# Kernel tuning notes

Hardware: AMD Instinct MI355X
Metric: run time of the kernel (lower is better)

Reference implementation:

```python
import jax, jax.numpy as jnp
import numpy as np

RADIUS, HEAD, SLOT, DIM = 16.0, 8, 112, 512

def _l2norm(x, axis):
    n = jnp.linalg.norm(x, axis=axis, keepdims=True)
    return x / jnp.maximum(n, 1e-12)

def _layernorm(x, g, b, eps=1e-5):
    mu = jnp.mean(x, axis=-1, keepdims=True)
    var = jnp.mean((x - mu) ** 2, axis=-1, keepdims=True)
    return (x - mu) / jnp.sqrt(var + eps) * g + b

def setup_inputs() -> dict:
    key = jax.random.key(0)
    ks = jax.random.split(key, 12)
    B, S = 32, 512
    return {
        "query": jax.random.normal(ks[0], (B, S, DIM), jnp.float32),
        "value": jax.random.normal(ks[1], (B, S, DIM), jnp.float32),
        "key_mem": jax.random.normal(ks[2], (HEAD * SLOT, DIM // HEAD), jnp.float32) * 0.5,
        "value_mem": jax.random.normal(ks[3], (SLOT, DIM), jnp.float32) * 0.5,
        "Wq": jax.random.normal(ks[4], (DIM, DIM), jnp.float32) * 0.02,
        "bq": jnp.zeros((DIM,), jnp.float32),
        "Wv": jax.random.normal(ks[5], (DIM, DIM), jnp.float32) * 0.02,
        "bv": jnp.zeros((DIM,), jnp.float32),
        "Wl": jax.random.normal(ks[6], (DIM, DIM * HEAD), jnp.float32) * 0.02,
        "bl": jnp.zeros((DIM,), jnp.float32),
        "g1": jnp.ones((DIM,), jnp.float32), "b1": jnp.zeros((DIM,), jnp.float32),
        "g2": jnp.ones((DIM,), jnp.float32), "b2": jnp.zeros((DIM,), jnp.float32),
        "g3": jnp.ones((DIM,), jnp.float32), "b3": jnp.zeros((DIM,), jnp.float32),
    }

def reference(query, value, key_mem, value_mem, Wq, bq, Wv, bv, Wl, bl,
              g1, b1, g2, b2, g3, b3):
    B, S, C = query.shape
    mq = query.reshape(B * S, C)                                   # (BS, 512)
    # --- key addressing (read path) ---
    key_norm = _l2norm(key_mem.reshape(HEAD, SLOT, -1), axis=2)    # (h, s, 64)
    eq = _l2norm((mq @ Wq.T + bq).reshape(B * S, HEAD, -1), axis=2)
    key_sim = jnp.einsum('bhd,hsd->bhs', eq, key_norm)             # (BS, h, s)
    key_add = jax.nn.softmax(RADIUS * key_sim, axis=2)
    m_head = jnp.einsum('bhs,sd->bhd', key_add,
                        jax.lax.stop_gradient(value_mem))          # (BS, h, 512)
    vir = _layernorm(m_head.reshape(B * S, HEAD * DIM) @ Wl.T + bl, g2, b2)
    te_fusion = _layernorm(query + vir.reshape(B, S, DIM), g1, b1)  # dropout = eval identity
    # --- value addressing (write/train path) ---
    mv = value.reshape(B * S, DIM)
    ev = jax.lax.stop_gradient(mv) @ Wv.T + bv
    value_norm = _l2norm(value_mem, axis=1)                        # (s, 512)
    value_sim = _l2norm(ev, axis=1) @ value_norm.T                 # (BS, s)
    value_add = jax.nn.softmax(RADIUS * value_sim, axis=1)
    aud = value_add @ value_mem                                    # (BS, 512)
    contrastive = 0.5 * jnp.abs(jnp.eye(SLOT, dtype=value_norm.dtype)
                                - value_norm @ value_norm.T).sum()[None]
    mvd = jax.lax.stop_gradient(mv)
    cos = (aud * mvd).sum(1) / jnp.maximum(
        jnp.linalg.norm(aud, axis=1) * jnp.linalg.norm(mvd, axis=1), 1e-8)
    recon = jnp.abs(1.0 - cos).reshape(B, S).sum(1)                # (B,)
    aud = _layernorm(aud, g3, b3)
    tr_fusion = _layernorm(query + aud.reshape(B, S, DIM), g1, b1)
    return (te_fusion, tr_fusion, recon, contrastive)
```

## Files before the change

kernel.cpp:

```cpp
#include <hip/hip_runtime.h>
#include <math.h>

#define DIMC   512
#define HEADS  8
#define SLOTS  112
#define HD     64
#define NROWS  16384
#define RADIUSF 16.0f

typedef short short8 __attribute__((ext_vector_type(8)));
typedef unsigned short ushort8 __attribute__((ext_vector_type(8)));
typedef float f32x4  __attribute__((ext_vector_type(4)));

__device__ __forceinline__ unsigned short f2bf(float f)
{
    unsigned u = __float_as_uint(f);
    unsigned r = (u + 0x7FFFu + ((u >> 16) & 1u)) >> 16;
    return (unsigned short)r;
}
__device__ __forceinline__ float bf2f(unsigned short h)
{
    return __uint_as_float((unsigned)h << 16);
}

__device__ __forceinline__ void gl16(const void* g, void* lds_wave_base)
{
    __builtin_amdgcn_global_load_lds(
        (const __attribute__((address_space(1))) unsigned int*)g,
        (__attribute__((address_space(3))) unsigned int*)lds_wave_base,
        16, 0, 0);
}

#define DPP_ADD(x, ctrl, rmask)                                               \
    (x) += __int_as_float(__builtin_amdgcn_update_dpp(                        \
               0, __float_as_int(x), (ctrl), (rmask), 0xf, true))

__device__ __forceinline__ float wsum64(float x)
{
    DPP_ADD(x, 0x111, 0xf);
    DPP_ADD(x, 0x112, 0xf);
    DPP_ADD(x, 0x114, 0xf);
    DPP_ADD(x, 0x118, 0xf);
    DPP_ADD(x, 0x142, 0xa);
    DPP_ADD(x, 0x143, 0xc);
    return __int_as_float(__builtin_amdgcn_readlane(__float_as_int(x), 63));
}

__device__ __forceinline__ void wsum64_4(float& a, float& b, float& c, float& d)
{
    DPP_ADD(a, 0x111, 0xf); DPP_ADD(b, 0x111, 0xf); DPP_ADD(c, 0x111, 0xf); DPP_ADD(d, 0x111, 0xf);
    DPP_ADD(a, 0x112, 0xf); DPP_ADD(b, 0x112, 0xf); DPP_ADD(c, 0x112, 0xf); DPP_ADD(d, 0x112, 0xf);
    DPP_ADD(a, 0x114, 0xf); DPP_ADD(b, 0x114, 0xf); DPP_ADD(c, 0x114, 0xf); DPP_ADD(d, 0x114, 0xf);
    DPP_ADD(a, 0x118, 0xf); DPP_ADD(b, 0x118, 0xf); DPP_ADD(c, 0x118, 0xf); DPP_ADD(d, 0x118, 0xf);
    DPP_ADD(a, 0x142, 0xa); DPP_ADD(b, 0x142, 0xa); DPP_ADD(c, 0x142, 0xa); DPP_ADD(d, 0x142, 0xa);
    DPP_ADD(a, 0x143, 0xc); DPP_ADD(b, 0x143, 0xc); DPP_ADD(c, 0x143, 0xc); DPP_ADD(d, 0x143, 0xc);
    a = __int_as_float(__builtin_amdgcn_readlane(__float_as_int(a), 63));
    b = __int_as_float(__builtin_amdgcn_readlane(__float_as_int(b), 63));
    c = __int_as_float(__builtin_amdgcn_readlane(__float_as_int(c), 63));
    d = __int_as_float(__builtin_amdgcn_readlane(__float_as_int(d), 63));
}

__global__ __launch_bounds__(256)
void gemm_bf16(const short* __restrict__ A, int lda,
               const short* __restrict__ B, int ldb,
               float* __restrict__ C, unsigned short* __restrict__ Cb,
               int ldc, int K, const float* __restrict__ bias, int Nvalid,
               int aZ, int bZ, int cZ)
{
    __shared__ short As[128 * 32];
    __shared__ short Bs[128 * 32];
    A += (size_t)blockIdx.z * aZ;
    B += (size_t)blockIdx.z * bZ;
    const size_t czoff = (size_t)blockIdx.z * cZ;
    const int tid  = threadIdx.x;
    const int wave = tid >> 6;
    const int lane = tid & 63;
    const int m0 = blockIdx.y * 128;
    const int n0 = blockIdx.x * 128;
    const int wm = (wave >> 1) * 64;
    const int wn = (wave & 1) * 64;

    const int srow = tid >> 2;
    const int schk = (tid & 3) * 8;

    const int fr = lane & 15;
    const int fq = (lane >> 4) * 8;

    f32x4 acc[4][4] = {};

    const short* Ag = A + (size_t)(m0 + srow) * lda + schk;
    const short* Bg = B + (size_t)(n0 + srow) * ldb + schk;

    short* asL = As + wave * 512;
    short* asU = As + 2048 + wave * 512;
    short* bsL = Bs + wave * 512;
    short* bsU = Bs + 2048 + wave * 512;

    for (int k0 = 0; k0 < K; k0 += 32) {
        gl16(Ag, asL);
        gl16(Ag + (size_t)64 * lda, asU);
        gl16(Bg, bsL);
        gl16(Bg + (size_t)64 * ldb, bsU);
        Ag += 32; Bg += 32;
        __syncthreads();
        short8 af[4], bf[4];
        #pragma unroll
        for (int i = 0; i < 4; ++i)
            af[i] = *(const short8*)&As[(wm + i * 16 + fr) * 32 + fq];
        #pragma unroll
        for (int j = 0; j < 4; ++j)
            bf[j] = *(const short8*)&Bs[(wn + j * 16 + fr) * 32 + fq];
        #pragma unroll
        for (int i = 0; i < 4; ++i)
            #pragma unroll
            for (int j = 0; j < 4; ++j)
                acc[i][j] = __builtin_amdgcn_mfma_f32_16x16x32_bf16(
                    af[i], bf[j], acc[i][j], 0, 0, 0);
        __syncthreads();
    }

    const int cr = (lane >> 4) * 4;
    const int cc = lane & 15;
    #pragma unroll
    for (int i = 0; i < 4; ++i) {
        const int grow = m0 + wm + i * 16 + cr;
        #pragma unroll
        for (int j = 0; j < 4; ++j) {
            const int gcol = n0 + wn + j * 16 + cc;
            if (gcol < Nvalid) {
                const float bb = bias ? bias[gcol] : 0.f;
                const size_t base = czoff + (size_t)grow * ldc + gcol;
                #pragma unroll
                for (int r = 0; r < 4; ++r) {
                    const float val = acc[i][j][r] + bb;
                    if (C)  C[base + (size_t)r * ldc]  = val;
                    if (Cb) Cb[base + (size_t)r * ldc] = f2bf(val);
                }
            }
        }
    }
}

__global__ __launch_bounds__(256)
void gemm_softmax(const short* __restrict__ A, int lda, int aZ,
                  const short* __restrict__ B, int ldb, int bZ,
                  int K,
                  unsigned short* __restrict__ Ob, int ldo, int oPerZ, int padN)
{
    __shared__ short As[128 * 32];
    __shared__ short Bs[128 * 32];
    __shared__ float P[128][113];
    __shared__ float hinvS[128];
    A += (size_t)blockIdx.z * aZ;
    B += (size_t)blockIdx.z * bZ;
    const int tid  = threadIdx.x;
    const int wave = tid >> 6;
    const int lane = tid & 63;
    const int m0 = blockIdx.y * 128;
    const int wm = (wave >> 1) * 64;
    const int wn = (wave & 1) * 64;
    const int srow = tid >> 2;
    const int schk = (tid & 3) * 8;
    const int fr = lane & 15;
    const int fq = (lane >> 4) * 8;

    f32x4 acc[4][4] = {};
    float ss[4] = {0.f, 0.f, 0.f, 0.f};

    const short* Ag = A + (size_t)(m0 + srow) * lda + schk;
    const short* Bg = B + (size_t)srow * ldb + schk;

    short* asL = As + wave * 512;
    short* asU = As + 2048 + wave * 512;
    short* bsL = Bs + wave * 512;
    short* bsU = Bs + 2048 + wave * 512;

    for (int k0 = 0; k0 < K; k0 += 32) {
        gl16(Ag, asL);
        gl16(Ag + (size_t)64 * lda, asU);
        gl16(Bg, bsL);
        gl16(Bg + (size_t)64 * ldb, bsU);
        Ag += 32; Bg += 32;
        __syncthreads();
        short8 af[4], bf[4];
        #pragma unroll
        for (int i = 0; i < 4; ++i)
            af[i] = *(const short8*)&As[(wm + i * 16 + fr) * 32 + fq];
        #pragma unroll
        for (int j = 0; j < 4; ++j)
            bf[j] = *(const short8*)&Bs[(wn + j * 16 + fr) * 32 + fq];
        #pragma unroll
        for (int i = 0; i < 4; ++i)
            #pragma unroll
            for (int e = 0; e < 8; ++e) {
                const float f = bf2f((unsigned short)af[i][e]);
                ss[i] += f * f;
            }
        #pragma unroll
        for (int i = 0; i < 4; ++i)
            #pragma unroll
            for (int j = 0; j < 4; ++j)
                acc[i][j] = __builtin_amdgcn_mfma_f32_16x16x32_bf16(
                    af[i], bf[j], acc[i][j], 0, 0, 0);
        __syncthreads();
    }

    #pragma unroll
    for (int i = 0; i < 4; ++i) {
        ss[i] += __shfl_xor(ss[i], 16, 64);
        ss[i] += __shfl_xor(ss[i], 32, 64);
    }
    if (lane < 16) {
        #pragma unroll
        for (int i = 0; i < 4; ++i)
            hinvS[wm + i * 16 + lane] = 1.f / fmaxf(sqrtf(ss[i]), 1e-12f);
    }

    const int cr = (lane >> 4) * 4;
    const int cc = lane & 15;
    #pragma unroll
    for (int i = 0; i < 4; ++i) {
        const int prow = wm + i * 16 + cr;
        #pragma unroll
        for (int j = 0; j < 4; ++j) {
            const int pcol = wn + j * 16 + cc;
            if (pcol < SLOTS) {
                #pragma unroll
                for (int r = 0; r < 4; ++r)
                    P[prow + r][pcol] = acc[i][j][r];
            }
        }
    }
    __syncthreads();

    const int rowt = tid >> 1;
    const int half = tid & 1;
    const int k0 = half * 56;
    const int rr = m0 + rowt;
    const float s = RADIUSF * hinvS[rowt];
    float mx = -1e30f;
    for (int k = k0; k < k0 + 56; ++k) mx = fmaxf(mx, P[rowt][k]);
    mx = fmaxf(mx, __shfl_xor(mx, 1, 64));
    float sum = 0.f;
    for (int k = k0; k < k0 + 56; ++k) {
        const float e = __expf(s * (P[rowt][k] - mx));
        P[rowt][k] = e;
        sum += e;
    }
    sum += __shfl_xor(sum, 1, 64);
    const float inv = 1.f / sum;
    unsigned short* orow = Ob + (size_t)rr * ldo + (size_t)blockIdx.z * oPerZ;
    for (int k = k0; k < k0 + 56; ++k) orow[k] = f2bf(P[rowt][k] * inv);
    if (half == 1)
        for (int k = SLOTS; k < padN; ++k) orow[k] = 0;
}

__global__ __launch_bounds__(512, 2)
void gemm_vir_te(const short* __restrict__ A, int lda,
                 const short* __restrict__ B, int ldb, int K,
                 const float* __restrict__ bias, const float* __restrict__ query,
                 const float* __restrict__ g1, const float* __restrict__ b1,
                 const float* __restrict__ g2, const float* __restrict__ b2,
                 float* __restrict__ out_te)
{
    __shared__ short As0[64 * 32];
    __shared__ short As1[64 * 32];
    __shared__ short Bs0[512 * 32];
    __shared__ short Bs1[512 * 32];
    __shared__ float parm[5 * 512];
    __shared__ float red1[128], red2[128];

    const int tid  = threadIdx.x;
    const int wave = tid >> 6;
    const int lane = tid & 63;
    const int m0 = blockIdx.x * 64;
    const int s = wave >> 1;
    const int h = wave & 1;
    const int fr = lane & 15;
    const int fq = (lane >> 4) * 8;

    parm[tid]        = bias[tid];
    parm[512 + tid]  = g2[tid];
    parm[1024 + tid] = b2[tid];
    parm[1536 + tid] = g1[tid];
    parm[2048 + tid] = b1[tid];

    f32x4 acc[16] = {};

    const int lrow = lane >> 2;
    const int lchk = (lane & 3) * 8;

    for (int k0 = 0; k0 < K; k0 += 64) {
        if (wave < 4)
            gl16(A + (size_t)(m0 + wave * 16 + lrow) * lda + k0 + lchk,
                 As0 + wave * 512);
        else
            gl16(A + (size_t)(m0 + (wave - 4) * 16 + lrow) * lda + k0 + 32 + lchk,
                 As1 + (wave - 4) * 512);
        #pragma unroll
        for (int s4 = 0; s4 < 4; ++s4) {
            const size_t br = (size_t)(wave * 64 + s4 * 16 + lrow);
            gl16(B + br * ldb + k0 + lchk,      Bs0 + (wave * 64 + s4 * 16) * 32);
            gl16(B + br * ldb + k0 + 32 + lchk, Bs1 + (wave * 64 + s4 * 16) * 32);
        }
        __syncthreads();
        const short8 af0 = *(const short8*)&As0[(s * 16 + fr) * 32 + fq];
        const short8 af1 = *(const short8*)&As1[(s * 16 + fr) * 32 + fq];
        #pragma unroll
        for (int c = 0; c < 16; ++c) {
            const short8 bf0 = *(const short8*)&Bs0[(h * 256 + c * 16 + fr) * 32 + fq];
            acc[c] = __builtin_amdgcn_mfma_f32_16x16x32_bf16(af0, bf0, acc[c], 0, 0, 0);
            const short8 bf1 = *(const short8*)&Bs1[(h * 256 + c * 16 + fr) * 32 + fq];
            acc[c] = __builtin_amdgcn_mfma_f32_16x16x32_bf16(af1, bf1, acc[c], 0, 0, 0);
        }
        __syncthreads();
    }

    const int cc = lane & 15;
    const int cr = (lane >> 4) * 4;
    const int rowb = s * 16 + cr;

    float s1[4] = {0.f, 0.f, 0.f, 0.f}, s2[4] = {0.f, 0.f, 0.f, 0.f};
    #pragma unroll
    for (int c = 0; c < 16; ++c) {
        const float blc = parm[h * 256 + c * 16 + cc];
        #pragma unroll
        for (int r = 0; r < 4; ++r) {
            const float x = acc[c][r] + blc;
            s1[r] += x;
            s2[r] += x * x;
        }
    }
    #pragma unroll
    for (int k = 1; k < 16; k <<= 1)
        #pragma unroll
        for (int r = 0; r < 4; ++r) {
            s1[r] += __shfl_xor(s1[r], k, 16);
            s2[r] += __shfl_xor(s2[r], k, 16);
        }
    if (cc == 0)
        #pragma unroll
        for (int r = 0; r < 4; ++r) {
            red1[(rowb + r) * 2 + h] = s1[r];
            red2[(rowb + r) * 2 + h] = s2[r];
        }
    __syncthreads();
    float mu[4], rs[4];
    #pragma unroll
    for (int r = 0; r < 4; ++r) {
        const float t1 = red1[(rowb + r) * 2] + red1[(rowb + r) * 2 + 1];
        const float t2 = red2[(rowb + r) * 2] + red2[(rowb + r) * 2 + 1];
        mu[r] = t1 * (1.f / DIMC);
        const float var = t2 * (1.f / DIMC) - mu[r] * mu[r];
        rs[r] = rsqrtf(var + 1e-5f);
    }
    __syncthreads();

    float t1[4] = {0.f, 0.f, 0.f, 0.f}, t2[4] = {0.f, 0.f, 0.f, 0.f};
    #pragma unroll
    for (int c = 0; c < 16; ++c) {
        const int col = h * 256 + c * 16 + cc;
        const float blc = parm[col];
        const float g2c = parm[512 + col];
        const float b2c = parm[1024 + col];
        #pragma unroll
        for (int r = 0; r < 4; ++r) {
            const float x = acc[c][r] + blc;
            const float qv = query[(size_t)(m0 + rowb + r) * DIMC + col];
            const float y = qv + (x - mu[r]) * rs[r] * g2c + b2c;
            t1[r] += y;
            t2[r] += y * y;
        }
    }
    #pragma unroll
    for (int k = 1; k < 16; k <<= 1)
        #pragma unroll
        for (int r = 0; r < 4; ++r) {
            t1[r] += __shfl_xor(t1[r], k, 16);
            t2[r] += __shfl_xor(t2[r], k, 16);
        }
    if (cc == 0)
        #pragma unroll
        for (int r = 0; r < 4; ++r) {
            red1[(rowb + r) * 2 + h] = t1[r];
            red2[(rowb + r) * 2 + h] = t2[r];
        }
    __syncthreads();
    float mu2[4], rs2[4];
    #pragma unroll
    for (int r = 0; r < 4; ++r) {
        const float u1 = red1[(rowb + r) * 2] + red1[(rowb + r) * 2 + 1];
        const float u2 = red2[(rowb + r) * 2] + red2[(rowb + r) * 2 + 1];
        mu2[r] = u1 * (1.f / DIMC);
        const float var = u2 * (1.f / DIMC) - mu2[r] * mu2[r];
        rs2[r] = rsqrtf(var + 1e-5f);
    }

    #pragma unroll
    for (int c = 0; c < 16; ++c) {
        const int col = h * 256 + c * 16 + cc;
        const float blc = parm[col];
        const float g2c = parm[512 + col];
        const float b2c = parm[1024 + col];
        const float g1c = parm[1536 + col];
        const float b1c = parm[2048 + col];
        #pragma unroll
        for (int r = 0; r < 4; ++r) {
            const float x = acc[c][r] + blc;
            const float qv = query[(size_t)(m0 + rowb + r) * DIMC + col];
            const float y = qv + (x - mu[r]) * rs[r] * g2c + b2c;
            out_te[(size_t)(m0 + rowb + r) * DIMC + col] =
                (y - mu2[r]) * rs2[r] * g1c + b1c;
        }
    }
}

#define FUSED_LDS_DECL                                                        \
    __shared__ float U[17408];    \
    float* P = U;                                                             \
    short* As0 = (short*)U;                             \
    short* As1 = As0 + 1024;                            \
    short* Bs0 = As1 + 1024;                           \
    short* Bs1 = Bs0 + 16384;

#define FUSED_GEMM_CORE(Aptr, lda, Bptr, ldb, K)                              \
    f32x4 acc[2][4] = {};                                                     \
    {                                                                         \
        const int lrow = lane >> 2;                                           \
        const int lchk = (lane & 3) * 8;                                      \
        for (int k0 = 0; k0 < (K); k0 += 64) {                                \
            if (wave < 2)                                                     \
                gl16((Aptr) + (size_t)(m0 + wave * 16 + lrow) * (lda) + k0 + lchk, \
                     As0 + wave * 512);                                       \
            else if (wave < 4)                                                \
                gl16((Aptr) + (size_t)(m0 + (wave - 2) * 16 + lrow) * (lda) + k0 + 32 + lchk, \
                     As1 + (wave - 2) * 512);                                 \
            _Pragma("unroll")                                                 \
            for (int s = 0; s < 4; ++s) {                                     \
                const size_t brow = (size_t)(wave * 64 + s * 16 + lrow);      \
                gl16((Bptr) + brow * (ldb) + k0 + lchk,                       \
                     Bs0 + (wave * 64 + s * 16) * 32);                        \
                gl16((Bptr) + brow * (ldb) + k0 + 32 + lchk,                  \
                     Bs1 + (wave * 64 + s * 16) * 32);                        \
            }                                                                 \
            __syncthreads();                                                  \
            short8 af0[2], af1[2], bf0[4], bf1[4];                            \
            _Pragma("unroll")                                                 \
            for (int i = 0; i < 2; ++i) {                                     \
                af0[i] = *(const short8*)&As0[(i * 16 + fr) * 32 + fq];       \
                af1[i] = *(const short8*)&As1[(i * 16 + fr) * 32 + fq];       \
            }                                                                 \
            _Pragma("unroll")                                                 \
            for (int c = 0; c < 4; ++c) {                                     \
                bf0[c] = *(const short8*)&Bs0[(wave * 64 + c * 16 + fr) * 32 + fq]; \
                bf1[c] = *(const short8*)&Bs1[(wave * 64 + c * 16 + fr) * 32 + fq]; \
            }                                                                 \
            _Pragma("unroll")                                                 \
            for (int i = 0; i < 2; ++i)                                       \
                _Pragma("unroll")                                             \
                for (int c = 0; c < 4; ++c) {                                 \
                    acc[i][c] = __builtin_amdgcn_mfma_f32_16x16x32_bf16(      \
                        af0[i], bf0[c], acc[i][c], 0, 0, 0);                  \
                    acc[i][c] = __builtin_amdgcn_mfma_f32_16x16x32_bf16(      \
                        af1[i], bf1[c], acc[i][c], 0, 0, 0);                  \
                }                                                             \
            __syncthreads();                                                  \
        }                                                                     \
    }                                                                         \
    {                                                                         \
        const int cr = (lane >> 4) * 4;                                       \
        const int cc = lane & 15;                                             \
        _Pragma("unroll")                                                     \
        for (int i = 0; i < 2; ++i)                                           \
            _Pragma("unroll")                                                 \
            for (int c = 0; c < 4; ++c) {                                     \
                const int col = wave * 64 + c * 16 + cc;                      \
                _Pragma("unroll")                                             \
                for (int r = 0; r < 4; ++r)                                   \
                    P[(i * 16 + cr + r) * 516 + col] = acc[i][c][r];          \
            }                                                                 \
    }                                                                         \
    __syncthreads();

__global__ __launch_bounds__(512, 4)
void gemm_aud_tr(const short* __restrict__ A, int lda,
                 const short* __restrict__ B, int ldb, int K,
                 const float* __restrict__ value, const float* __restrict__ query,
                 const float* __restrict__ g1, const float* __restrict__ b1,
                 const float* __restrict__ g3, const float* __restrict__ b3,
                 float* __restrict__ out_tr, float* __restrict__ recon)
{
    FUSED_LDS_DECL
    __shared__ float red[8];
    const int tid = threadIdx.x;
    const int wave = tid >> 6;
    const int lane = tid & 63;
    const int m0 = blockIdx.x * 32;
    const int fr = lane & 15;
    const int fq = (lane >> 4) * 8;

    FUSED_GEMM_CORE(A, lda, B, ldb, K)

    const int c0 = lane * 8;
    float gg3[8], bb3[8], gg1[8], bb1[8];
    *(f32x4*)&gg3[0] = *(const f32x4*)(g3 + c0);
    *(f32x4*)&gg3[4] = *(const f32x4*)(g3 + c0 + 4);
    *(f32x4*)&bb3[0] = *(const f32x4*)(b3 + c0);
    *(f32x4*)&bb3[4] = *(const f32x4*)(b3 + c0 + 4);
    *(f32x4*)&gg1[0] = *(const f32x4*)(g1 + c0);
    *(f32x4*)&gg1[4] = *(const f32x4*)(g1 + c0 + 4);
    *(f32x4*)&bb1[0] = *(const f32x4*)(b1 + c0);
    *(f32x4*)&bb1[4] = *(const f32x4*)(b1 + c0 + 4);

    float rloc = 0.f;
    for (int rp = 0; rp < 2; ++rp) {
        const int lr0 = wave * 4 + rp * 2;
        float a[2][8], v[2][8], q[2][8];
        #pragma unroll
        for (int p = 0; p < 2; ++p) {
            *(f32x4*)&a[p][0] = *(const f32x4*)&P[(lr0 + p) * 516 + c0];
            *(f32x4*)&a[p][4] = *(const f32x4*)&P[(lr0 + p) * 516 + c0 + 4];
            const size_t gbase = (size_t)(m0 + lr0 + p) * DIMC + c0;
            *(f32x4*)&v[p][0] = *(const f32x4*)(value + gbase);
            *(f32x4*)&v[p][4] = *(const f32x4*)(value + gbase + 4);
            *(f32x4*)&q[p][0] = *(const f32x4*)(query + gbase);
            *(f32x4*)&q[p][4] = *(const f32x4*)(query + gbase + 4);
        }
        float dot[2] = {0.f, 0.f}, na[2] = {0.f, 0.f};
        float nv[2] = {0.f, 0.f}, s1[2] = {0.f, 0.f};
        #pragma unroll
        for (int p = 0; p < 2; ++p)
            #pragma unroll
            for (int j = 0; j < 8; ++j) {
                dot[p] += a[p][j] * v[p][j];
                na[p]  += a[p][j] * a[p][j];
                nv[p]  += v[p][j] * v[p][j];
                s1[p]  += a[p][j];
            }
        wsum64_4(dot[0], na[0], nv[0], s1[0]);
        wsum64_4(dot[1], na[1], nv[1], s1[1]);

        #pragma unroll
        for (int p = 0; p < 2; ++p) {
            const float cosv = dot[p] / fmaxf(sqrtf(na[p]) * sqrtf(nv[p]), 1e-8f);
            rloc += fabsf(1.f - cosv);
        }

        float y[2][8];
        float t1[2] = {0.f, 0.f}, t2[2] = {0.f, 0.f};
        #pragma unroll
        for (int p = 0; p < 2; ++p) {
            const float mu = s1[p] * (1.f / DIMC);
            const float var = na[p] * (1.f / DIMC) - mu * mu;
            const float rstd = rsqrtf(var + 1e-5f);
            #pragma unroll
            for (int j = 0; j < 8; ++j) {
                const float w = (a[p][j] - mu) * rstd * gg3[j] + bb3[j];
                y[p][j] = q[p][j] + w;
                t1[p] += y[p][j];
                t2[p] += y[p][j] * y[p][j];
            }
        }
        wsum64_4(t1[0], t2[0], t1[1], t2[1]);

        #pragma unroll
        for (int p = 0; p < 2; ++p) {
            const float mu = t1[p] * (1.f / DIMC);
            const float var = t2[p] * (1.f / DIMC) - mu * mu;
            const float rstd = rsqrtf(var + 1e-5f);
            float o[8];
            #pragma unroll
            for (int j = 0; j < 8; ++j)
                o[j] = (y[p][j] - mu) * rstd * gg1[j] + bb1[j];
            const size_t gbase = (size_t)(m0 + lr0 + p) * DIMC + c0;
            *(float4*)(out_tr + gbase)     = make_float4(o[0], o[1], o[2], o[3]);
            *(float4*)(out_tr + gbase + 4) = make_float4(o[4], o[5], o[6], o[7]);
        }
    }

    if (lane == 0) red[wave] = rloc;
    __syncthreads();
    if (tid == 0)
        atomicAdd(&recon[m0 >> 9], red[0] + red[1] + red[2] + red[3]
                                 + red[4] + red[5] + red[6] + red[7]);
}

__device__ __forceinline__ float block_sum_256(float v, float* red)
{
    #pragma unroll
    for (int off = 32; off; off >>= 1) v += __shfl_down(v, off, 64);
    const int lane = threadIdx.x & 63, wid = threadIdx.x >> 6;
    __syncthreads();
    if (lane == 0) red[wid] = v;
    __syncthreads();
    return red[0] + red[1] + red[2] + red[3];
}

__global__ void conv_all(const float* __restrict__ q, const float* __restrict__ v,
                         const float* __restrict__ Wq, const float* __restrict__ Wv,
                         const float* __restrict__ Wl, const float* __restrict__ vm,
                         unsigned short* __restrict__ qbf, unsigned short* __restrict__ vbf,
                         unsigned short* __restrict__ wqbf, unsigned short* __restrict__ wvbf,
                         unsigned short* __restrict__ wlbf, unsigned short* __restrict__ vmbf)
{
    const int i = blockIdx.x * blockDim.x + threadIdx.x;
    const float* src;
    unsigned short* dst;
    int off;
    if (i < 2097152)      { src = q;  dst = qbf;  off = i; }
    else if (i < 4194304) { src = v;  dst = vbf;  off = i - 2097152; }
    else if (i < 4259840) { src = Wq; dst = wqbf; off = i - 4194304; }
    else if (i < 4325376) { src = Wv; dst = wvbf; off = i - 4259840; }
    else if (i < 4849664) { src = Wl; dst = wlbf; off = i - 4325376; }
    else if (i < 4864000) { src = vm; dst = vmbf; off = i - 4849664; }
    else {
        const int j = i - 4864000;
        *(ushort4*)(vmbf + 57344 + (size_t)j * 4) = make_ushort4(0, 0, 0, 0);
        return;
    }
    const float4 x = *(const float4*)(src + (size_t)off * 4);
    ushort4 o;
    o.x = f2bf(x.x); o.y = f2bf(x.y); o.z = f2bf(x.z); o.w = f2bf(x.w);
    *(ushort4*)(dst + (size_t)off * 4) = o;
}

__global__ void prep_key_norm(const float* __restrict__ km,
                              unsigned short* __restrict__ knb,
                              float* __restrict__ outrc)
{
    const int row = blockIdx.x;
    const int h = row >> 7, s = row & 127;
    const int lane = threadIdx.x;
    if (row == 0 && lane < 33) outrc[lane] = 0.f;
    const float v = (s < SLOTS) ? km[(size_t)(h * SLOTS + s) * HD + lane] : 0.f;
    const float ssum = wsum64(v * v);
    const float inv = 1.f / fmaxf(sqrtf(ssum), 1e-12f);
    knb[(size_t)row * HD + lane] = f2bf(v * inv);
}

__global__ void prep_value_norm(const float* __restrict__ vm,
                                float* __restrict__ vn,
                                unsigned short* __restrict__ vnb,
                                unsigned short* __restrict__ vmTb)
{
    const int row = blockIdx.x;
    const int tid = threadIdx.x;
    if (row >= 112) {
        const int idx = (row - 112) * 256 + tid;
        if (idx < 8192) {
            vmTb[(size_t)(idx >> 4) * 128 + 112 + (idx & 15)] = 0;
        } else {
            const int j = idx - 8192;
            vnb[(size_t)(112 + (j >> 9)) * 512 + (j & 511)] = 0;
        }
        return;
    }
    __shared__ float red[4];
    const float v0 = vm[(size_t)row * DIMC + tid];
    const float v1 = vm[(size_t)row * DIMC + 256 + tid];
    const float tot = block_sum_256(v0 * v0 + v1 * v1, red);
    const float inv = 1.f / fmaxf(sqrtf(tot), 1e-12f);
    vn[(size_t)row * DIMC + tid]        = v0 * inv;
    vn[(size_t)row * DIMC + 256 + tid]  = v1 * inv;
    vnb[(size_t)row * DIMC + tid]       = f2bf(v0 * inv);
    vnb[(size_t)row * DIMC + 256 + tid] = f2bf(v1 * inv);
    vmTb[(size_t)tid * 128 + row]         = f2bf(v0);
    vmTb[(size_t)(256 + tid) * 128 + row] = f2bf(v1);
}

__global__ void contrastive_kernel(const float* __restrict__ vn, float* __restrict__ outc)
{
    __shared__ float vni[DIMC];
    __shared__ float red[2];
    const int i = blockIdx.x, tid = threadIdx.x;
    for (int d = tid; d < DIMC; d += 128) vni[d] = vn[(size_t)i * DIMC + d];
    __syncthreads();
    float t = 0.f;
    if (tid < SLOTS) {
        const float* r = vn + (size_t)tid * DIMC;
        float dot = 0.f;
        for (int d = 0; d < DIMC; ++d) dot += vni[d] * r[d];
        const float delta = (tid == i) ? 1.f : 0.f;
        t = fabsf(delta - dot);
    }
    #pragma unroll
    for (int off = 32; off; off >>= 1) t += __shfl_down(t, off, 64);
    if ((tid & 63) == 0) red[tid >> 6] = t;
    __syncthreads();
    if (tid == 0) atomicAdd(outc, 0.5f * (red[0] + red[1]));
}

extern "C" void kernel_launch(void* const* d_in, const int* in_sizes, int n_in,
                              void* d_out, int out_size, void* d_ws, size_t ws_size,
                              hipStream_t stream)
{
    const float* query = (const float*)d_in[0];
    const float* value = (const float*)d_in[1];
    const float* keym  = (const float*)d_in[2];
    const float* vmem  = (const float*)d_in[3];
    const float* Wq    = (const float*)d_in[4];
    const float* bq    = (const float*)d_in[5];
    const float* Wv    = (const float*)d_in[6];
    const float* bv    = (const float*)d_in[7];
    const float* Wl    = (const float*)d_in[8];
    const float* bl    = (const float*)d_in[9];
    const float* g1    = (const float*)d_in[10];
    const float* b1    = (const float*)d_in[11];
    const float* g2    = (const float*)d_in[12];
    const float* b2    = (const float*)d_in[13];
    const float* g3    = (const float*)d_in[14];
    const float* b3    = (const float*)d_in[15];

    float* out    = (float*)d_out;
    float* out_te = out;
    float* out_tr = out + 8388608;
    float* out_rc = out + 16777216;

    float* ws = (float*)d_ws;
    unsigned short* w_knb  = (unsigned short*)(ws + 0);
    unsigned short* w_vmTb = (unsigned short*)(ws + 32768);
    unsigned short* w_vnb  = (unsigned short*)(ws + 65536);
    float*          w_vn   = ws + 98304;
    unsigned short* w_w2tbf= (unsigned short*)(ws + 155648);
    unsigned short* w_vmbf = (unsigned short*)(ws + 385024);
    unsigned short* w_wlbf = (unsigned short*)(ws + 417792);
    unsigned short* w_xbf  = (unsigned short*)(ws + 1466368);
    unsigned short* w_kaddc= (unsigned short*)(ws + 5660672);
    unsigned short* w_vsb  = (unsigned short*)(ws + 13000704);
    unsigned short* w_qbf  = (unsigned short*)(ws + 14049280);
    unsigned short* w_vbf  = (unsigned short*)(ws + 18243584);
    unsigned short* w_wqbf = (unsigned short*)(ws + 22437888);
    unsigned short* w_wvbf = (unsigned short*)(ws + 22568960);

    conv_all<<<19008, 256, 0, stream>>>(query, value, Wq, Wv, Wl, vmem,
                                        w_qbf, w_vbf, w_wqbf, w_wvbf,
                                        w_wlbf, w_vmbf);
    prep_key_norm<<<1024, 64, 0, stream>>>(keym, w_knb, out_rc);
    prep_value_norm<<<176, 256, 0, stream>>>(vmem, w_vn, w_vnb, w_vmTb);
    contrastive_kernel<<<112, 128, 0, stream>>>(w_vn, out_rc + 32);
    gemm_bf16<<<dim3(1, 4, 8), 256, 0, stream>>>(
        (const short*)w_wlbf, HEADS * DIMC, (const short*)w_vmbf, DIMC,
        nullptr, w_w2tbf, HEADS * SLOTS, DIMC, nullptr, SLOTS,
        DIMC, 0, SLOTS);

    gemm_bf16<<<dim3(4, 128), 256, 0, stream>>>(
        (const short*)w_qbf, DIMC, (const short*)w_wqbf, DIMC,
        nullptr, w_xbf, DIMC, DIMC, bq, DIMC, 0, 0, 0);
    gemm_softmax<<<dim3(1, 128, 8), 256, 0, stream>>>(
        (const short*)w_xbf, DIMC, HD, (const short*)w_knb, HD, 128 * HD,
        HD, w_kaddc, HEADS * SLOTS, SLOTS, SLOTS);
    gemm_vir_te<<<NROWS / 64, 512, 0, stream>>>(
        (const short*)w_kaddc, HEADS * SLOTS, (const short*)w_w2tbf, HEADS * SLOTS,
        HEADS * SLOTS, bl, query, g1, b1, g2, b2, out_te);

    gemm_bf16<<<dim3(4, 128), 256, 0, stream>>>(
        (const short*)w_vbf, DIMC, (const short*)w_wvbf, DIMC,
        nullptr, w_xbf, DIMC, DIMC, bv, DIMC, 0, 0, 0);
    gemm_softmax<<<dim3(1, 128, 1), 256, 0, stream>>>(
        (const short*)w_xbf, DIMC, 0, (const short*)w_vnb, DIMC, 0,
        DIMC, w_vsb, 128, 0, 128);
    gemm_aud_tr<<<NROWS / 32, 512, 0, stream>>>(
        (const short*)w_vsb, 128, (const short*)w_vmTb, 128, 128,
        value, query, g1, b1, g3, b3, out_tr, out_rc);
}
```

Before: 341.2 us.

## Double gemm_vir_te block to 1024 threads and alias params into B tile LDS

The vir/te GEMM+double-layernorm kernel now launches 1024 threads per block with 16 waves, each owning a 16x128 output slice instead of 16x256. This halves per-wave accumulator registers and the per-wave share of B-tile loads. The layernorm parameter buffer now reuses the B-tile LDS after the K loop rather than a separate allocation, which lowers LDS use. The costs are four-way cross-wave reduction partials, an extra barrier, and a launch bound of (1024,4) that may force register spills.

```diff
diff --git a/kernel.cpp b/kernel.cpp
--- a/kernel.cpp
+++ b/kernel.cpp
@@ -255,7 +255,7 @@
         for (int k = SLOTS; k < padN; ++k) orow[k] = 0;
 }
 
-__global__ __launch_bounds__(512, 2)
+__global__ __launch_bounds__(1024, 4)
 void gemm_vir_te(const short* __restrict__ A, int lda,
                  const short* __restrict__ B, int ldb, int K,
                  const float* __restrict__ bias, const float* __restrict__ query,
@@ -267,25 +267,19 @@
     __shared__ short As1[64 * 32];
     __shared__ short Bs0[512 * 32];
     __shared__ short Bs1[512 * 32];
-    __shared__ float parm[5 * 512];
-    __shared__ float red1[128], red2[128];
+    __shared__ float red1[256], red2[256];
+    float* parm = (float*)Bs0;
 
     const int tid  = threadIdx.x;
     const int wave = tid >> 6;
     const int lane = tid & 63;
     const int m0 = blockIdx.x * 64;
-    const int s = wave >> 1;
-    const int h = wave & 1;
+    const int s = wave >> 2;
+    const int h = wave & 3;
     const int fr = lane & 15;
     const int fq = (lane >> 4) * 8;
 
-    parm[tid]        = bias[tid];
-    parm[512 + tid]  = g2[tid];
-    parm[1024 + tid] = b2[tid];
-    parm[1536 + tid] = g1[tid];
-    parm[2048 + tid] = b1[tid];
-
-    f32x4 acc[16] = {};
+    f32x4 acc[8] = {};
 
     const int lrow = lane >> 2;
     const int lchk = (lane & 3) * 8;
@@ -294,27 +288,38 @@
         if (wave < 4)
             gl16(A + (size_t)(m0 + wave * 16 + lrow) * lda + k0 + lchk,
                  As0 + wave * 512);
-        else
+        else if (wave < 8)
             gl16(A + (size_t)(m0 + (wave - 4) * 16 + lrow) * lda + k0 + 32 + lchk,
                  As1 + (wave - 4) * 512);
         #pragma unroll
-        for (int s4 = 0; s4 < 4; ++s4) {
-            const size_t br = (size_t)(wave * 64 + s4 * 16 + lrow);
-            gl16(B + br * ldb + k0 + lchk,      Bs0 + (wave * 64 + s4 * 16) * 32);
-            gl16(B + br * ldb + k0 + 32 + lchk, Bs1 + (wave * 64 + s4 * 16) * 32);
+        for (int g = 0; g < 2; ++g) {
+            const size_t br = (size_t)(wave * 32 + g * 16 + lrow);
+            gl16(B + br * ldb + k0 + lchk,      Bs0 + (wave * 32 + g * 16) * 32);
+            gl16(B + br * ldb + k0 + 32 + lchk, Bs1 + (wave * 32 + g * 16) * 32);
         }
         __syncthreads();
         const short8 af0 = *(const short8*)&As0[(s * 16 + fr) * 32 + fq];
         const short8 af1 = *(const short8*)&As1[(s * 16 + fr) * 32 + fq];
         #pragma unroll
-        for (int c = 0; c < 16; ++c) {
-            const short8 bf0 = *(const short8*)&Bs0[(h * 256 + c * 16 + fr) * 32 + fq];
+        for (int c = 0; c < 8; ++c) {
+            const short8 bf0 = *(const short8*)&Bs0[(h * 128 + c * 16 + fr) * 32 + fq];
             acc[c] = __builtin_amdgcn_mfma_f32_16x16x32_bf16(af0, bf0, acc[c], 0, 0, 0);
-            const short8 bf1 = *(const short8*)&Bs1[(h * 256 + c * 16 + fr) * 32 + fq];
+            const short8 bf1 = *(const short8*)&Bs1[(h * 128 + c * 16 + fr) * 32 + fq];
             acc[c] = __builtin_amdgcn_mfma_f32_16x16x32_bf16(af1, bf1, acc[c], 0, 0, 0);
         }
         __syncthreads();
     }
+
+    if (tid < 512) {
+        parm[tid]        = bias[tid];
+        parm[512 + tid]  = g2[tid];
+        parm[1024 + tid] = b2[tid];
+    } else {
+        const int t = tid - 512;
+        parm[1536 + t] = g1[t];
+        parm[2048 + t] = b1[t];
+    }
+    __syncthreads();
 
     const int cc = lane & 15;
     const int cr = (lane >> 4) * 4;
@@ -322,8 +327,8 @@
 
     float s1[4] = {0.f, 0.f, 0.f, 0.f}, s2[4] = {0.f, 0.f, 0.f, 0.f};
     #pragma unroll
-    for (int c = 0; c < 16; ++c) {
-        const float blc = parm[h * 256 + c * 16 + cc];
+    for (int c = 0; c < 8; ++c) {
+        const float blc = parm[h * 128 + c * 16 + cc];
         #pragma unroll
         for (int r = 0; r < 4; ++r) {
             const float x = acc[c][r] + blc;
@@ -341,15 +346,17 @@
     if (cc == 0)
         #pragma unroll
         for (int r = 0; r < 4; ++r) {
-            red1[(rowb + r) * 2 + h] = s1[r];
-            red2[(rowb + r) * 2 + h] = s2[r];
+            red1[(rowb + r) * 4 + h] = s1[r];
+            red2[(rowb + r) * 4 + h] = s2[r];
         }
     __syncthreads();
     float mu[4], rs[4];
     #pragma unroll
     for (int r = 0; r < 4; ++r) {
-        const float t1 = red1[(rowb + r) * 2] + red1[(rowb + r) * 2 + 1];
-        const float t2 = red2[(rowb + r) * 2] + red2[(rowb + r) * 2 + 1];
+        const float t1 = red1[(rowb + r) * 4] + red1[(rowb + r) * 4 + 1]
+                       + red1[(rowb + r) * 4 + 2] + red1[(rowb + r) * 4 + 3];
+        const float t2 = red2[(rowb + r) * 4] + red2[(rowb + r) * 4 + 1]
+                       + red2[(rowb + r) * 4 + 2] + red2[(rowb + r) * 4 + 3];
         mu[r] = t1 * (1.f / DIMC);
         const float var = t2 * (1.f / DIMC) - mu[r] * mu[r];
         rs[r] = rsqrtf(var + 1e-5f);
@@ -358,8 +365,8 @@
 
     float t1[4] = {0.f, 0.f, 0.f, 0.f}, t2[4] = {0.f, 0.f, 0.f, 0.f};
     #pragma unroll
-    for (int c = 0; c < 16; ++c) {
-        const int col = h * 256 + c * 16 + cc;
+    for (int c = 0; c < 8; ++c) {
+        const int col = h * 128 + c * 16 + cc;
         const float blc = parm[col];
         const float g2c = parm[512 + col];
         const float b2c = parm[1024 + col];
@@ -382,23 +389,25 @@
     if (cc == 0)
         #pragma unroll
         for (int r = 0; r < 4; ++r) {
-            red1[(rowb + r) * 2 + h] = t1[r];
-            red2[(rowb + r) * 2 + h] = t2[r];
+            red1[(rowb + r) * 4 + h] = t1[r];
+            red2[(rowb + r) * 4 + h] = t2[r];
         }
     __syncthreads();
     float mu2[4], rs2[4];
     #pragma unroll
     for (int r = 0; r < 4; ++r) {
-        const float u1 = red1[(rowb + r) * 2] + red1[(rowb + r) * 2 + 1];
-        const float u2 = red2[(rowb + r) * 2] + red2[(rowb + r) * 2 + 1];
+        const float u1 = red1[(rowb + r) * 4] + red1[(rowb + r) * 4 + 1]
+                       + red1[(rowb + r) * 4 + 2] + red1[(rowb + r) * 4 + 3];
+        const float u2 = red2[(rowb + r) * 4] + red2[(rowb + r) * 4 + 1]
+                       + red2[(rowb + r) * 4 + 2] + red2[(rowb + r) * 4 + 3];
         mu2[r] = u1 * (1.f / DIMC);
         const float var = u2 * (1.f / DIMC) - mu2[r] * mu2[r];
         rs2[r] = rsqrtf(var + 1e-5f);
     }
 
     #pragma unroll
-    for (int c = 0; c < 16; ++c) {
-        const int col = h * 256 + c * 16 + cc;
+    for (int c = 0; c < 8; ++c) {
+        const int col = h * 128 + c * 16 + cc;
         const float blc = parm[col];
         const float g2c = parm[512 + col];
         const float b2c = parm[1024 + col];
@@ -749,7 +758,7 @@
     gemm_softmax<<<dim3(1, 128, 8), 256, 0, stream>>>(
         (const short*)w_xbf, DIMC, HD, (const short*)w_knb, HD, 128 * HD,
         HD, w_kaddc, HEADS * SLOTS, SLOTS, SLOTS);
-    gemm_vir_te<<<NROWS / 64, 512, 0, stream>>>(
+    gemm_vir_te<<<NROWS / 64, 1024, 0, stream>>>(
         (const short*)w_kaddc, HEADS * SLOTS, (const short*)w_w2tbf, HEADS * SLOTS,
         HEADS * SLOTS, bl, query, g1, b1, g2, b2, out_te);
 
```

Result: no change. 344.7 us (+1.0%).
